# Kernel tuning notes

Hardware: AMD Instinct MI355X
Metric: run time of the kernel (lower is better)

Reference implementation:

```python
import jax, jax.numpy as jnp
import numpy as np

B, SQ, SK, D, H, DFF, L = 8, 1024, 1024, 512, 8, 2048, 2
HD = D // H  # head dim = 64
EPS = 1e-5


def _ln(x, g, b):
    mu = jnp.mean(x, axis=-1, keepdims=True)
    var = jnp.mean((x - mu) ** 2, axis=-1, keepdims=True)
    return (x - mu) * jax.lax.rsqrt(var + EPS) * g + b


def setup_inputs() -> dict:
    key = jax.random.key(0)
    ks = jax.random.split(key, 16)
    std = 0.02
    inp = {
        'q': jax.random.normal(ks[0], (B, SQ, D), jnp.float32),
        'k': jax.random.normal(ks[1], (B, SK, D), jnp.float32),
        'v': jax.random.normal(ks[2], (B, SK, D), jnp.float32),
        # per-layer stacked params (weights stored [in, out])
        'WQ': jax.random.normal(ks[3], (L, D, D), jnp.float32) * std,
        'bQ': jnp.zeros((L, D), jnp.float32),
        'WK': jax.random.normal(ks[4], (L, D, D), jnp.float32) * std,
        'bK': jnp.zeros((L, D), jnp.float32),
        'WV': jax.random.normal(ks[5], (L, D, D), jnp.float32) * std,
        'bV': jnp.zeros((L, D), jnp.float32),
        'WO': jax.random.normal(ks[6], (L, D, D), jnp.float32) * std,
        'bO': jnp.zeros((L, D), jnp.float32),
        'Wf1': jax.random.normal(ks[7], (L, D, DFF), jnp.float32) * std,
        'bf1': jnp.zeros((L, DFF), jnp.float32),
        'Wf2': jax.random.normal(ks[8], (L, DFF, D), jnp.float32) * std,
        'bf2': jnp.zeros((L, D), jnp.float32),
        'ln1_g': jnp.ones((L, D), jnp.float32),
        'ln1_b': jnp.zeros((L, D), jnp.float32),
        'ln2_g': jnp.ones((L, D), jnp.float32),
        'ln2_b': jnp.zeros((L, D), jnp.float32),
        'scale': jnp.full((L,), HD ** -0.5, jnp.float32),       # self.scale init
        'extra_scale': jnp.ones((L,), jnp.float32),             # self.extra_scale init
        'gate_attn': jnp.ones((L,), jnp.float32),
        'gate_ffn': jnp.ones((L,), jnp.float32),
    }
    return inp


def reference(q, k, v, WQ, bQ, WK, bK, WV, bV, WO, bO, Wf1, bf1, Wf2, bf2,
              ln1_g, ln1_b, ln2_g, ln2_b, scale, extra_scale, gate_attn, gate_ffn):
    prev = None  # Realformer residual attention scores
    for i in range(L):
        # QKV projections -> [B, H, S, HD]
        qh = (jnp.einsum('bsd,de->bse', q, WQ[i]) + bQ[i]).reshape(B, SQ, H, HD).transpose(0, 2, 1, 3)
        kh = (jnp.einsum('bsd,de->bse', k, WK[i]) + bK[i]).reshape(B, SK, H, HD).transpose(0, 2, 1, 3)
        vh = (jnp.einsum('bsd,de->bse', v, WV[i]) + bV[i]).reshape(B, SK, H, HD).transpose(0, 2, 1, 3)
        eff_scale = scale[i] * jnp.clip(extra_scale[i], 0.01, 50.0)
        scores = jnp.einsum('bhqd,bhkd->bhqk', qh, kh) * eff_scale  # [B,H,SQ,SK]
        if prev is not None:
            scores = scores + prev
        attn = jax.nn.softmax(scores, axis=-1)
        out = jnp.einsum('bhqk,bhkd->bhqd', attn, vh)
        out = out.transpose(0, 2, 1, 3).reshape(B, SQ, D)
        out = jnp.einsum('bsd,de->bse', out, WO[i]) + bO[i]
        # gated residual + post-norm
        q = q + jax.nn.softplus(gate_attn[i]) * out
        q = _ln(q, ln1_g[i], ln1_b[i])
        # FFN (exact gelu like torch default)
        ff = jax.nn.gelu(jnp.einsum('bsd,df->bsf', q, Wf1[i]) + bf1[i], approximate=False)
        ff = jnp.einsum('bsf,fd->bsd', ff, Wf2[i]) + bf2[i]
        q = q + jax.nn.softplus(gate_ffn[i]) * ff
        q = _ln(q, ln2_g[i], ln2_b[i])
        prev = scores
    return q
```

## Files before the change

### kernel.cpp

```cpp
#include <hip/hip_runtime.h>

#define B_   8
#define SQ_  1024
#define SK_  1024
#define D_   512
#define H_   8
#define DFF_ 2048
#define L_   2
#define HD_  64
#define M_   8192

typedef __bf16 bf16;
using bf16x8 = __attribute__((ext_vector_type(8))) __bf16;
using f32x4  = __attribute__((ext_vector_type(4))) float;

__device__ inline f32x4 mfma16(bf16x8 a, bf16x8 b, f32x4 c) {
  return __builtin_amdgcn_mfma_f32_16x16x32_bf16(a, b, c, 0, 0, 0);
}

__device__ __forceinline__ void gl2lds16(const bf16* g, bf16* l) {
  __builtin_amdgcn_global_load_lds(
      (const __attribute__((address_space(1))) void*)g,
      (__attribute__((address_space(3))) void*)l, 16, 0, 0);
}

__device__ __forceinline__ float gelu_fast(float x) {
  float u = 1.5957691216f * (x + 0.044715f * x * x * x);
  return x / (1.0f + __expf(-u));
}

struct TP4 { const float* in[4]; bf16* out[4]; };
__global__ __launch_bounds__(256) void transpose4_k(TP4 p) {
  __shared__ bf16 tile[32][33];
  int z = blockIdx.z, wsel = z >> 1, l = z & 1;
  const float* inp  = p.in[wsel]  + (size_t)l * D_ * D_;
  bf16*        outp = p.out[wsel] + (size_t)l * D_ * D_;
  int c0 = blockIdx.x * 32, r0 = blockIdx.y * 32;
  int tx = threadIdx.x & 31, ty = threadIdx.x >> 5;
#pragma unroll
  for (int i = 0; i < 32; i += 8)
    tile[ty + i][tx] = (bf16)inp[(size_t)(r0 + ty + i) * D_ + c0 + tx];
  __syncthreads();
#pragma unroll
  for (int i = 0; i < 32; i += 8)
    outp[(size_t)(c0 + ty + i) * D_ + r0 + tx] = tile[tx][ty + i];
}

__global__ __launch_bounds__(256) void transpose_k(
    const float* __restrict__ in, bf16* __restrict__ out, int R, int C) {
  __shared__ bf16 tile[32][33];
  const float* inp  = in  + (size_t)blockIdx.z * R * C;
  bf16*        outp = out + (size_t)blockIdx.z * R * C;
  int c0 = blockIdx.x * 32, r0 = blockIdx.y * 32;
  int tx = threadIdx.x & 31, ty = threadIdx.x >> 5;
#pragma unroll
  for (int i = 0; i < 32; i += 8)
    tile[ty + i][tx] = (bf16)inp[(size_t)(r0 + ty + i) * C + c0 + tx];
  __syncthreads();
#pragma unroll
  for (int i = 0; i < 32; i += 8)
    outp[(size_t)(c0 + ty + i) * R + r0 + tx] = tile[tx][ty + i];
}

__global__ __launch_bounds__(256) void f2b3_k(
    const float* __restrict__ a, const float* __restrict__ b,
    const float* __restrict__ c, bf16* __restrict__ oa,
    bf16* __restrict__ ob, bf16* __restrict__ oc) {
  int which = blockIdx.y;
  const float* in = (which == 0) ? a : (which == 1) ? b : c;
  bf16* out = (which == 0) ? oa : (which == 1) ? ob : oc;
  int i = (blockIdx.x * 256 + threadIdx.x) * 4;
  float4 v = *(const float4*)&in[i];
  out[i] = (bf16)v.x; out[i + 1] = (bf16)v.y;
  out[i + 2] = (bf16)v.z; out[i + 3] = (bf16)v.w;
}

struct G256 { const bf16* A; const bf16* Bt; const float* bias; bf16* C; };

#define MFB(mh) \
  _Pragma("unroll") \
  for (int mi = 0; mi < 4; mi++) { \
    _Pragma("unroll") \
    for (int ni = 0; ni < 4; ni++) \
      acc[(mh) * 4 + mi][ni] = mfma16(a[mi], b[ni], acc[(mh) * 4 + mi][ni]); \
  }

#define PHASE(s, mh, STAGE, VM) \
  { \
    if ((mh) == 0) { \
      a[0] = ldA(s, 0); a[1] = ldA(s, 1); a[2] = ldA(s, 2); a[3] = ldA(s, 3); \
      b[0] = ldB(s, 0); b[1] = ldB(s, 1); b[2] = ldB(s, 2); b[3] = ldB(s, 3); \
    } else { \
      a[0] = ldA(s, 4); a[1] = ldA(s, 5); a[2] = ldA(s, 6); a[3] = ldA(s, 7); \
    } \
    STAGE; \
    VM; \
    __builtin_amdgcn_s_barrier(); \
    asm volatile("s_waitcnt lgkmcnt(0)" ::: "memory"); \
    __builtin_amdgcn_sched_barrier(0); \
    __builtin_amdgcn_s_setprio(1); \
    MFB(mh); \
    __builtin_amdgcn_s_setprio(0); \
    __builtin_amdgcn_s_barrier(); \
  }

__global__ __launch_bounds__(512, 2) void gemm256_k(G256 g0, G256 g1,
                                                    int Nsz, int Ksz,
                                                    int gelu) {
  __shared__ bf16 As[4 * 8192];
  __shared__ bf16 Bs[4 * 8192];
  const G256 g = blockIdx.z ? g1 : g0;
  const int tid = threadIdx.x;
  const int w = tid >> 6, lane = tid & 63;
  const int quad = lane >> 4, l16 = lane & 15;
  const int wm = w >> 2, wn = w & 3;
  const int m0 = blockIdx.x * 256, n0 = blockIdx.y * 256;
  const int NCH = Ksz >> 5;
  const int ITERS = NCH >> 2;

  const int srow = tid >> 2;
  const int ssw = ((tid & 3) ^ (srow & 3) ^ ((srow >> 2) & 3)) << 3;
  const int swr = ((quad ^ (l16 & 3) ^ (l16 >> 2)) << 3);

  auto stageA = [&](int kc, int s) {
    const bf16* gp = g.A + (size_t)(m0 + srow) * Ksz + kc * 32 + ssw;
    gl2lds16(gp, &As[s * 8192 + w * 512]);
    gl2lds16(gp + (size_t)128 * Ksz, &As[s * 8192 + 4096 + w * 512]);
  };
  auto stageB = [&](int kc, int s) {
    const bf16* gp = g.Bt + (size_t)(n0 + srow) * Ksz + kc * 32 + ssw;
    gl2lds16(gp, &Bs[s * 8192 + w * 512]);
    gl2lds16(gp + (size_t)128 * Ksz, &Bs[s * 8192 + 4096 + w * 512]);
  };
  auto ldA = [&](int s, int mi) {
    return *(const bf16x8*)&As[s * 8192 + (wm * 128 + mi * 16 + l16) * 32 + swr];
  };
  auto ldB = [&](int s, int ni) {
    return *(const bf16x8*)&Bs[s * 8192 + (wn * 64 + ni * 16 + l16) * 32 + swr];
  };

  f32x4 acc[8][4] = {};

  stageA(0, 0); stageB(0, 0);
  stageA(1, 1); stageB(1, 1);
  stageA(2, 2); stageB(2, 2);
  asm volatile("s_waitcnt vmcnt(4)" ::: "memory");
  __builtin_amdgcn_s_barrier();

  for (int it = 0; it < ITERS; ++it) {
    const int c = it * 4;
    const bool last = (it + 1 == ITERS);
    bf16x8 a[4], b[4];
    PHASE(0, 0, stageA(c + 3, 3), )
    PHASE(0, 1, stageB(c + 3, 3), )
    PHASE(1, 0, if (!last) stageA(c + 4, 0), )
    PHASE(1, 1, if (!last) stageB(c + 4, 0),
          if (!last) { asm volatile("s_waitcnt vmcnt(4)" ::: "memory"); }
          else { asm volatile("s_waitcnt vmcnt(0)" ::: "memory"); })
    PHASE(2, 0, if (!last) stageA(c + 5, 1), )
    PHASE(2, 1, if (!last) stageB(c + 5, 1), )
    PHASE(3, 0, if (!last) stageA(c + 6, 2), )
    PHASE(3, 1, if (!last) stageB(c + 6, 2),
          asm volatile("s_waitcnt vmcnt(4)" ::: "memory"))
  }

#pragma unroll
  for (int mi = 0; mi < 8; mi++)
#pragma unroll
    for (int ni = 0; ni < 4; ni++) {
      const int col = n0 + wn * 64 + ni * 16 + l16;
      const float bv = g.bias[col];
#pragma unroll
      for (int r = 0; r < 4; r++) {
        const int row = m0 + wm * 128 + mi * 16 + quad * 4 + r;
        float x = acc[mi][ni][r] + bv;
        if (gelu) x = gelu_fast(x);
        g.C[(size_t)row * Nsz + col] = (bf16)x;
      }
    }
}

__global__ __launch_bounds__(512, 2) void gemm256s_k(
    const bf16* __restrict__ A, const bf16* __restrict__ Bt,
    bf16* __restrict__ P, int Nsz, int Kstride, int Kpart) {
  __shared__ bf16 As[4 * 8192];
  __shared__ bf16 Bs[4 * 8192];
  const int z = blockIdx.z;
  const int koff = z * Kpart;
  const int tid = threadIdx.x;
  const int w = tid >> 6, lane = tid & 63;
  const int quad = lane >> 4, l16 = lane & 15;
  const int wm = w >> 2, wn = w & 3;
  const int m0 = blockIdx.x * 256, n0 = blockIdx.y * 256;
  const int ITERS = (Kpart >> 5) >> 2;

  const int srow = tid >> 2;
  const int ssw = ((tid & 3) ^ (srow & 3) ^ ((srow >> 2) & 3)) << 3;
  const int swr = ((quad ^ (l16 & 3) ^ (l16 >> 2)) << 3);

  auto stageA = [&](int kc, int s) {
    const bf16* gp = A + (size_t)(m0 + srow) * Kstride + koff + kc * 32 + ssw;
    gl2lds16(gp, &As[s * 8192 + w * 512]);
    gl2lds16(gp + (size_t)128 * Kstride, &As[s * 8192 + 4096 + w * 512]);
  };
  auto stageB = [&](int kc, int s) {
    const bf16* gp = Bt + (size_t)(n0 + srow) * Kstride + koff + kc * 32 + ssw;
    gl2lds16(gp, &Bs[s * 8192 + w * 512]);
    gl2lds16(gp + (size_t)128 * Kstride, &Bs[s * 8192 + 4096 + w * 512]);
  };
  auto ldA = [&](int s, int mi) {
    return *(const bf16x8*)&As[s * 8192 + (wm * 128 + mi * 16 + l16) * 32 + swr];
  };
  auto ldB = [&](int s, int ni) {
    return *(const bf16x8*)&Bs[s * 8192 + (wn * 64 + ni * 16 + l16) * 32 + swr];
  };

  f32x4 acc[8][4] = {};

  stageA(0, 0); stageB(0, 0);
  stageA(1, 1); stageB(1, 1);
  stageA(2, 2); stageB(2, 2);
  asm volatile("s_waitcnt vmcnt(4)" ::: "memory");
  __builtin_amdgcn_s_barrier();

  for (int it = 0; it < ITERS; ++it) {
    const int c = it * 4;
    const bool last = (it + 1 == ITERS);
    bf16x8 a[4], b[4];
    PHASE(0, 0, stageA(c + 3, 3), )
    PHASE(0, 1, stageB(c + 3, 3), )
    PHASE(1, 0, if (!last) stageA(c + 4, 0), )
    PHASE(1, 1, if (!last) stageB(c + 4, 0),
          if (!last) { asm volatile("s_waitcnt vmcnt(4)" ::: "memory"); }
          else { asm volatile("s_waitcnt vmcnt(0)" ::: "memory"); })
    PHASE(2, 0, if (!last) stageA(c + 5, 1), )
    PHASE(2, 1, if (!last) stageB(c + 5, 1), )
    PHASE(3, 0, if (!last) stageA(c + 6, 2), )
    PHASE(3, 1, if (!last) stageB(c + 6, 2),
          asm volatile("s_waitcnt vmcnt(4)" ::: "memory"))
  }

  const size_t Msz = (size_t)gridDim.x * 256;
  bf16* Pz = P + (size_t)z * Msz * Nsz;
#pragma unroll
  for (int mi = 0; mi < 8; mi++)
#pragma unroll
    for (int ni = 0; ni < 4; ni++) {
      const int col = n0 + wn * 64 + ni * 16 + l16;
#pragma unroll
      for (int r = 0; r < 4; r++) {
        const int row = m0 + wm * 128 + mi * 16 + quad * 4 + r;
        Pz[(size_t)row * Nsz + col] = (bf16)acc[mi][ni][r];
      }
    }
}

__global__ __launch_bounds__(512, 2) void gemm128_k(
    const bf16* __restrict__ A, const bf16* __restrict__ Bt,
    const float* __restrict__ bias, bf16* __restrict__ Cb,
    float* __restrict__ Cf, int Nsz, int Ksz) {
  __shared__ bf16 As[4 * 4096];
  __shared__ bf16 Bs[4 * 4096];
  const int tid = threadIdx.x;
  const int w = tid >> 6, lane = tid & 63;
  const int quad = lane >> 4, l16 = lane & 15;
  const int wm = w >> 2, wn = w & 3;
  const int m0 = blockIdx.x * 128, n0 = blockIdx.y * 128;
  const int NCH = Ksz >> 5;

  const int srow = tid >> 2;
  const int ssw = ((tid & 3) ^ (srow & 3) ^ ((srow >> 2) & 3)) << 3;
  const int swr = ((quad ^ (l16 & 3) ^ (l16 >> 2)) << 3);

  auto stageChunk = [&](int kc) {
    const int s = kc & 3;
    gl2lds16(A + (size_t)(m0 + srow) * Ksz + kc * 32 + ssw,
             &As[s * 4096 + w * 512]);
    gl2lds16(Bt + (size_t)(n0 + srow) * Ksz + kc * 32 + ssw,
             &Bs[s * 4096 + w * 512]);
  };
  auto ldA = [&](int s, int mi) {
    return *(const bf16x8*)&As[s * 4096 + (wm * 64 + mi * 16 + l16) * 32 + swr];
  };
  auto ldB = [&](int s, int ni) {
    return *(const bf16x8*)&Bs[s * 4096 + (wn * 32 + ni * 16 + l16) * 32 + swr];
  };

  f32x4 acc[4][2] = {};

  stageChunk(0); stageChunk(1); stageChunk(2);
  asm volatile("s_waitcnt vmcnt(4)" ::: "memory");
  __builtin_amdgcn_s_barrier();

  auto phase = [&](int c, int vml) {
    const int s = c & 3;
    if (vml == 4) stageChunk(c + 3);
    bf16x8 a0 = ldA(s, 0), a1 = ldA(s, 1), a2 = ldA(s, 2), a3 = ldA(s, 3);
    bf16x8 b0 = ldB(s, 0), b1 = ldB(s, 1);
    if (vml == 4)      asm volatile("s_waitcnt vmcnt(4)" ::: "memory");
    else if (vml == 2) asm volatile("s_waitcnt vmcnt(2)" ::: "memory");
    else if (vml == 0) asm volatile("s_waitcnt vmcnt(0)" ::: "memory");
    __builtin_amdgcn_s_barrier();
    asm volatile("s_waitcnt lgkmcnt(0)" ::: "memory");
    __builtin_amdgcn_sched_barrier(0);
    __builtin_amdgcn_s_setprio(1);
    acc[0][0] = mfma16(a0, b0, acc[0][0]);
    acc[0][1] = mfma16(a0, b1, acc[0][1]);
    acc[1][0] = mfma16(a1, b0, acc[1][0]);
    acc[1][1] = mfma16(a1, b1, acc[1][1]);
    acc[2][0] = mfma16(a2, b0, acc[2][0]);
    acc[2][1] = mfma16(a2, b1, acc[2][1]);
    acc[3][0] = mfma16(a3, b0, acc[3][0]);
    acc[3][1] = mfma16(a3, b1, acc[3][1]);
    __builtin_amdgcn_s_setprio(0);
    __builtin_amdgcn_s_barrier();
  };

  for (int c = 0; c + 4 <= NCH; ++c) phase(c, 4);
  phase(NCH - 3, 2);
  phase(NCH - 2, 0);
  phase(NCH - 1, -1);

#pragma unroll
  for (int mi = 0; mi < 4; mi++)
#pragma unroll
    for (int ni = 0; ni < 2; ni++) {
      const int col = n0 + wn * 32 + ni * 16 + l16;
      const float bv = bias[col];
#pragma unroll
      for (int r = 0; r < 4; r++) {
        const int row = m0 + wm * 64 + mi * 16 + quad * 4 + r;
        float x = acc[mi][ni][r] + bv;
        size_t idx = (size_t)row * Nsz + col;
        if (Cb) Cb[idx] = (bf16)x;
        if (Cf) Cf[idx] = x;
      }
    }
}

__global__ __launch_bounds__(256) void vtrans2_k(const bf16* __restrict__ vhh,
                                                 bf16* __restrict__ vt0,
                                                 bf16* __restrict__ vt1) {
  __shared__ bf16 sm[64][72];
  int kt = blockIdx.x, bh = blockIdx.y, z = blockIdx.z;
  int coloff = z ? D_ : 0;
  bf16* vt = z ? vt1 : vt0;
  int b = bh >> 3, h = bh & 7;
  int tid = threadIdx.x;
  for (int c = tid; c < 512; c += 256) {
    int key = c >> 3, off = (c & 7) * 8;
    *(uint4*)&sm[key][off] = *(const uint4*)
        &vhh[(size_t)(b * SK_ + kt * 64 + key) * (2 * D_) + coloff + h * 64 + off];
  }
  __syncthreads();
  for (int c = tid; c < 512; c += 256) {
    int hd = c >> 3, koff = (c & 7) * 8;
    bf16 tmp[8];
#pragma unroll
    for (int j = 0; j < 8; j++) tmp[j] = sm[koff + j][hd];
    *(uint4*)&vt[(size_t)(bh * 64 + hd) * SK_ + kt * 64 + koff] = *(uint4*)tmp;
  }
}

template<bool HAS0>
__global__ __launch_bounds__(256) void attn_t(
    const bf16* __restrict__ qh, const bf16* __restrict__ qh0,
    const bf16* __restrict__ kh, const bf16* __restrict__ kh0, int kstride,
    const bf16* __restrict__ vt, const float* __restrict__ scale,
    const float* __restrict__ extra, int li, bf16* __restrict__ ctx) {
  __shared__ bf16 Ks[2 * 2 * 2048];
  __shared__ bf16 K0s[HAS0 ? 2 * 2 * 2048 : 64];
  __shared__ bf16 Vs[2 * 2 * 2048];
  __shared__ bf16 Ps[4][16 * 72];
  int qt = blockIdx.x, bh = blockIdx.y;
  int b = bh >> 3, h = bh & 7;
  int tid = threadIdx.x, w = tid >> 6, lane = tid & 63;
  int quad = lane >> 4, l16 = lane & 15;
  const int r4 = lane >> 2;
  const int c4s = (((lane & 3) ^ (r4 & 3) ^ ((r4 >> 2) & 3))) * 8;
  const int swr = ((quad ^ (l16 & 3) ^ (l16 >> 2)) << 3);
  float eff1 = scale[li] * fminf(fmaxf(extra[li], 0.01f), 50.0f);
  float eff0 = HAS0 ? scale[li - 1] * fminf(fmaxf(extra[li - 1], 0.01f), 50.0f) : 0.f;
  bf16x8 aq[2][2], aq0[2][2];
#pragma unroll
  for (int mi = 0; mi < 2; mi++) {
    int qrow = b * SQ_ + qt * 128 + w * 32 + mi * 16 + l16;
    const bf16* qp = qh + (size_t)qrow * D_ + h * 64 + quad * 8;
    aq[mi][0] = *(const bf16x8*)qp; aq[mi][1] = *(const bf16x8*)(qp + 32);
#pragma unroll
    for (int k2 = 0; k2 < 2; k2++)
#pragma unroll
      for (int j = 0; j < 8; j++)
        aq[mi][k2][j] = (bf16)((float)aq[mi][k2][j] * eff1);
    if constexpr (HAS0) {
      const bf16* qp0 = qh0 + (size_t)qrow * D_ + h * 64 + quad * 8;
      aq0[mi][0] = *(const bf16x8*)qp0; aq0[mi][1] = *(const bf16x8*)(qp0 + 32);
#pragma unroll
      for (int k2 = 0; k2 < 2; k2++)
#pragma unroll
        for (int j = 0; j < 8; j++)
          aq0[mi][k2][j] = (bf16)((float)aq0[mi][k2][j] * eff0);
    }
  }
  bf16x8 ones;
#pragma unroll
  for (int j = 0; j < 8; j++) ones[j] = (bf16)1.0f;

  f32x4 o[2][4] = {};
  f32x4 ol[2] = {};

  auto stage = [&](int kt, int bufi) {
    size_t kg = (size_t)(b * SK_ + kt * 64 + w * 16 + r4) * kstride + h * 64 + c4s;
    gl2lds16(&kh[kg],      &Ks[(bufi * 2 + 0) * 2048 + (w * 16) * 32]);
    gl2lds16(&kh[kg + 32], &Ks[(bufi * 2 + 1) * 2048 + (w * 16) * 32]);
    if constexpr (HAS0) {
      gl2lds16(&kh0[kg],      &K0s[(bufi * 2 + 0) * 2048 + (w * 16) * 32]);
      gl2lds16(&kh0[kg + 32], &K0s[(bufi * 2 + 1) * 2048 + (w * 16) * 32]);
    }
    size_t vg = (size_t)(bh * 64 + w * 16 + r4) * SK_ + kt * 64 + c4s;
    gl2lds16(&vt[vg],      &Vs[(bufi * 2 + 0) * 2048 + (w * 16) * 32]);
    gl2lds16(&vt[vg + 32], &Vs[(bufi * 2 + 1) * 2048 + (w * 16) * 32]);
  };

  stage(0, 0);
  __syncthreads();
  int buf = 0;
  for (int kt = 0; kt < SK_ / 64; kt++, buf ^= 1) {
    if (kt + 1 < SK_ / 64) stage(kt + 1, buf ^ 1);
    bf16x8 bv[2][4];
#pragma unroll
    for (int kk = 0; kk < 2; kk++)
#pragma unroll
      for (int ni = 0; ni < 4; ni++)
        bv[kk][ni] = *(const bf16x8*)&Vs[kk * 2048 + buf * 4096 +
                                         (ni * 16 + l16) * 32 + swr];
#pragma unroll
    for (int mi = 0; mi < 2; mi++) {
#pragma unroll
      for (int ni = 0; ni < 4; ni++) {
        int ro = (ni * 16 + l16) * 32 + swr;
        f32x4 t = {};
        __builtin_amdgcn_s_setprio(1);
        t = mfma16(aq[mi][0], *(const bf16x8*)&Ks[0 * 2048 + buf * 4096 + ro], t);
        t = mfma16(aq[mi][1], *(const bf16x8*)&Ks[1 * 2048 + buf * 4096 + ro], t);
        if constexpr (HAS0) {
          t = mfma16(aq0[mi][0], *(const bf16x8*)&K0s[0 * 2048 + buf * 4096 + ro], t);
          t = mfma16(aq0[mi][1], *(const bf16x8*)&K0s[1 * 2048 + buf * 4096 + ro], t);
        }
        __builtin_amdgcn_s_setprio(0);
#pragma unroll
        for (int r = 0; r < 4; r++)
          Ps[w][(quad * 4 + r) * 72 + ni * 16 + l16] = (bf16)__expf(t[r]);
      }
#pragma unroll
      for (int kk = 0; kk < 2; kk++) {
        bf16x8 ap = *(const bf16x8*)&Ps[w][l16 * 72 + kk * 32 + quad * 8];
        __builtin_amdgcn_s_setprio(1);
        ol[mi] = mfma16(ap, ones, ol[mi]);
#pragma unroll
        for (int ni = 0; ni < 4; ni++)
          o[mi][ni] = mfma16(ap, bv[kk][ni], o[mi][ni]);
        __builtin_amdgcn_s_setprio(0);
      }
    }
    __syncthreads();
  }
#pragma unroll
  for (int mi = 0; mi < 2; mi++)
#pragma unroll
    for (int ni = 0; ni < 4; ni++)
#pragma unroll
      for (int r = 0; r < 4; r++) {
        int row = b * SQ_ + qt * 128 + w * 32 + mi * 16 + quad * 4 + r;
        ctx[(size_t)row * D_ + h * 64 + ni * 16 + l16] =
            (bf16)(o[mi][ni][r] / ol[mi][r]);
      }
}

__global__ __launch_bounds__(256) void ln_k(
    const float* __restrict__ cur_in, const float* __restrict__ add,
    const float* __restrict__ gate, const float* __restrict__ g,
    const float* __restrict__ bb, float* __restrict__ outf,
    bf16* __restrict__ outb) {
  int row = blockIdx.x, tid = threadIdx.x;
  float gv = gate[0];
  float sp = gv > 20.f ? gv : log1pf(expf(gv));
  size_t base = (size_t)row * D_;
  int c0 = tid * 2;
  float2 c2 = *(const float2*)&cur_in[base + c0];
  float2 a2 = *(const float2*)&add[base + c0];
  float x0 = c2.x + sp * a2.x, x1 = c2.y + sp * a2.y;
  float s = x0 + x1, s2 = x0 * x0 + x1 * x1;
#pragma unroll
  for (int m = 1; m < 64; m <<= 1) {
    s += __shfl_xor(s, m);
    s2 += __shfl_xor(s2, m);
  }
  __shared__ float sa[4], sb[4];
  int w = tid >> 6;
  if ((tid & 63) == 0) { sa[w] = s; sb[w] = s2; }
  __syncthreads();
  s = sa[0] + sa[1] + sa[2] + sa[3];
  s2 = sb[0] + sb[1] + sb[2] + sb[3];
  float mu = s * (1.f / D_);
  float var = s2 * (1.f / D_) - mu * mu;
  float rs = rsqrtf(var + 1e-5f);
  float y0 = (x0 - mu) * rs * g[c0] + bb[c0];
  float y1 = (x1 - mu) * rs * g[c0 + 1] + bb[c0 + 1];
  if (outf) { float2 y; y.x = y0; y.y = y1; *(float2*)&outf[base + c0] = y; }
  if (outb) { outb[base + c0] = (bf16)y0; outb[base + c0 + 1] = (bf16)y1; }
}

__global__ __launch_bounds__(256) void ln4_k(
    const float* __restrict__ cur_in, const bf16* __restrict__ P,
    const float* __restrict__ bias2, const float* __restrict__ gate,
    const float* __restrict__ g, const float* __restrict__ bb,
    float* __restrict__ outf, bf16* __restrict__ outb) {
  int row = blockIdx.x, tid = threadIdx.x;
  float gv = gate[0];
  float sp = gv > 20.f ? gv : log1pf(expf(gv));
  size_t base = (size_t)row * D_;
  int c0 = tid * 2;
  float2 c2 = *(const float2*)&cur_in[base + c0];
  float a0 = bias2[c0], a1 = bias2[c0 + 1];
  const size_t MD = (size_t)M_ * D_;
#pragma unroll
  for (int z = 0; z < 4; z++) {
    const bf16* pp = P + z * MD + base + c0;
    a0 += (float)pp[0];
    a1 += (float)pp[1];
  }
  float x0 = c2.x + sp * a0, x1 = c2.y + sp * a1;
  float s = x0 + x1, s2 = x0 * x0 + x1 * x1;
#pragma unroll
  for (int m = 1; m < 64; m <<= 1) {
    s += __shfl_xor(s, m);
    s2 += __shfl_xor(s2, m);
  }
  __shared__ float sa[4], sb[4];
  int w = tid >> 6;
  if ((tid & 63) == 0) { sa[w] = s; sb[w] = s2; }
  __syncthreads();
  s = sa[0] + sa[1] + sa[2] + sa[3];
  s2 = sb[0] + sb[1] + sb[2] + sb[3];
  float mu = s * (1.f / D_);
  float var = s2 * (1.f / D_) - mu * mu;
  float rs = rsqrtf(var + 1e-5f);
  float y0 = (x0 - mu) * rs * g[c0] + bb[c0];
  float y1 = (x1 - mu) * rs * g[c0 + 1] + bb[c0 + 1];
  if (outf) { float2 y; y.x = y0; y.y = y1; *(float2*)&outf[base + c0] = y; }
  if (outb) { outb[base + c0] = (bf16)y0; outb[base + c0 + 1] = (bf16)y1; }
}

extern "C" void kernel_launch(void* const* d_in, const int* in_sizes, int n_in,
                              void* d_out, int out_size, void* d_ws,
                              size_t ws_size, hipStream_t stream) {
  const float* qin = (const float*)d_in[0];
  const float* kin = (const float*)d_in[1];
  const float* vin = (const float*)d_in[2];
  const float* WQ  = (const float*)d_in[3];
  const float* bQ  = (const float*)d_in[4];
  const float* WK  = (const float*)d_in[5];
  const float* bK  = (const float*)d_in[6];
  const float* WV  = (const float*)d_in[7];
  const float* bV  = (const float*)d_in[8];
  const float* WO  = (const float*)d_in[9];
  const float* bO  = (const float*)d_in[10];
  const float* Wf1 = (const float*)d_in[11];
  const float* bf1 = (const float*)d_in[12];
  const float* Wf2 = (const float*)d_in[13];
  const float* bf2 = (const float*)d_in[14];
  const float* l1g = (const float*)d_in[15];
  const float* l1b = (const float*)d_in[16];
  const float* l2g = (const float*)d_in[17];
  const float* l2b = (const float*)d_in[18];
  const float* sc  = (const float*)d_in[19];
  const float* ex  = (const float*)d_in[20];
  const float* ga  = (const float*)d_in[21];
  const float* gf  = (const float*)d_in[22];

  char* p = (char*)d_ws;
  auto alloc = [&](size_t bytes) {
    void* r = (void*)p;
    p += (bytes + 255) & ~(size_t)255;
    return r;
  };
  bf16* WQt  = (bf16*)alloc((size_t)L_ * D_ * D_ * 2);
  bf16* WKt  = (bf16*)alloc((size_t)L_ * D_ * D_ * 2);
  bf16* WVt  = (bf16*)alloc((size_t)L_ * D_ * D_ * 2);
  bf16* WOt  = (bf16*)alloc((size_t)L_ * D_ * D_ * 2);
  bf16* Wf1t = (bf16*)alloc((size_t)L_ * D_ * DFF_ * 2);
  bf16* Wf2t = (bf16*)alloc((size_t)L_ * D_ * DFF_ * 2);
  float* cur  = (float*)alloc((size_t)M_ * D_ * 4);
  bf16* curb  = (bf16*)alloc((size_t)M_ * D_ * 2);
  bf16* qb    = (bf16*)alloc((size_t)M_ * D_ * 2);
  bf16* kb    = (bf16*)alloc((size_t)M_ * D_ * 2);
  bf16* vb    = (bf16*)alloc((size_t)M_ * D_ * 2);
  bf16* khh   = (bf16*)alloc((size_t)M_ * 2 * D_ * 2);
  bf16* vhh   = (bf16*)alloc((size_t)M_ * 2 * D_ * 2);
  bf16* qh0b  = (bf16*)alloc((size_t)M_ * D_ * 2);
  bf16* qh1b  = (bf16*)alloc((size_t)M_ * D_ * 2);
  bf16* vt0   = (bf16*)alloc((size_t)M_ * D_ * 2);
  bf16* vt1   = (bf16*)alloc((size_t)M_ * D_ * 2);
  bf16* ctx   = (bf16*)alloc((size_t)M_ * D_ * 2);
  float* proj  = (float*)alloc((size_t)M_ * D_ * 4);
  float* ffout = (float*)alloc((size_t)M_ * D_ * 4);
  bf16* parts  = (bf16*)proj;
  bf16* ffmid  = (bf16*)alloc((size_t)M_ * DFF_ * 2);
  (void)ffout;

  TP4 tp; tp.in[0] = WQ; tp.in[1] = WK; tp.in[2] = WV; tp.in[3] = WO;
  tp.out[0] = WQt; tp.out[1] = WKt; tp.out[2] = WVt; tp.out[3] = WOt;
  transpose4_k<<<dim3(16, 16, 8), 256, 0, stream>>>(tp);
  transpose_k<<<dim3(DFF_ / 32, D_ / 32, L_), 256, 0, stream>>>(Wf1, Wf1t, D_, DFF_);
  transpose_k<<<dim3(D_ / 32, DFF_ / 32, L_), 256, 0, stream>>>(Wf2, Wf2t, DFF_, D_);
  f2b3_k<<<dim3((M_ * D_) / 1024, 3), 256, 0, stream>>>(qin, kin, vin, qb, kb, vb);

  G256 gk; gk.A = kb; gk.Bt = WKt; gk.bias = bK; gk.C = khh;
  G256 gvv; gvv.A = vb; gvv.Bt = WVt; gvv.bias = bV; gvv.C = vhh;
  gemm256_k<<<dim3(M_ / 256, (2 * D_) / 256, 2), 512, 0, stream>>>(
      gk, gvv, 2 * D_, D_, 0);
  vtrans2_k<<<dim3(SK_ / 64, B_ * H_, 2), 256, 0, stream>>>(vhh, vt0, vt1);
  gemm128_k<<<dim3(M_ / 128, 4), 512, 0, stream>>>(
      qb, WQt, bQ, qh0b, nullptr, D_, D_);

  for (int li = 0; li < L_; li++) {
    if (li > 0)
      gemm128_k<<<dim3(M_ / 128, 4), 512, 0, stream>>>(
          curb, WQt + (size_t)li * D_ * D_, bQ + li * D_, qh1b, nullptr, D_, D_);
    if (li == 0)
      attn_t<false><<<dim3(SQ_ / 128, B_ * H_), 256, 0, stream>>>(
          qh0b, qh0b, khh, khh, 2 * D_, vt0, sc, ex, 0, ctx);
    else
      attn_t<true><<<dim3(SQ_ / 128, B_ * H_), 256, 0, stream>>>(
          qh1b, qh0b, khh + (size_t)li * D_, khh, 2 * D_, vt1, sc, ex, 1, ctx);
    gemm128_k<<<dim3(M_ / 128, 4), 512, 0, stream>>>(
        ctx, WOt + (size_t)li * D_ * D_, bO + li * D_, nullptr, proj, D_, D_);
    ln_k<<<M_, 256, 0, stream>>>((li == 0) ? qin : cur, proj, ga + li,
                                 l1g + li * D_, l1b + li * D_, cur, curb);
    G256 gf1; gf1.A = curb; gf1.Bt = Wf1t + (size_t)li * D_ * DFF_;
    gf1.bias = bf1 + li * DFF_; gf1.C = ffmid;
    gemm256_k<<<dim3(M_ / 256, DFF_ / 256, 1), 512, 0, stream>>>(
        gf1, gf1, DFF_, D_, 1);
    gemm256s_k<<<dim3(M_ / 256, D_ / 256, 4), 512, 0, stream>>>(
        ffmid, Wf2t + (size_t)li * DFF_ * D_, parts, D_, DFF_, DFF_ / 4);
    ln4_k<<<M_, 256, 0, stream>>>(cur, parts, bf2 + li * D_, gf + li,
                                  l2g + li * D_, l2b + li * D_,
                                  (li == L_ - 1) ? (float*)d_out : cur,
                                  (li == L_ - 1) ? nullptr : curb);
  }
}
```

Baseline: 506.7 us.

## Shrink attention tiles to 64 query rows and 32-key steps

The attention kernel now handles 64 query rows per block (16 per wave) instead of 128, and steps through keys 32 at a time instead of 64. This doubles the grid, halves per-wave accumulator registers, and cuts LDS use. The aim is higher occupancy and better CU fill. In exchange, K/V tiles are reused across fewer query rows, there are twice as many sync steps, the XOR swizzle is dropped (possible LDS bank conflicts), and the setprio hints are removed.

New measurement: 498.1 us. About the same (-1.7%).

```diff
diff --git a/kernel.cpp b/kernel.cpp
--- a/kernel.cpp
+++ b/kernel.cpp
@@ -368,113 +368,106 @@
     const bf16* __restrict__ kh, const bf16* __restrict__ kh0, int kstride,
     const bf16* __restrict__ vt, const float* __restrict__ scale,
     const float* __restrict__ extra, int li, bf16* __restrict__ ctx) {
-  __shared__ bf16 Ks[2 * 2 * 2048];
-  __shared__ bf16 K0s[HAS0 ? 2 * 2 * 2048 : 64];
-  __shared__ bf16 Vs[2 * 2 * 2048];
-  __shared__ bf16 Ps[4][16 * 72];
+  __shared__ bf16 Ks[2 * 2048];
+  __shared__ bf16 K0s[HAS0 ? 2 * 2048 : 64];
+  __shared__ bf16 Vs[2 * 2048];
+  __shared__ bf16 Ps[4][16 * 40];
   int qt = blockIdx.x, bh = blockIdx.y;
   int b = bh >> 3, h = bh & 7;
   int tid = threadIdx.x, w = tid >> 6, lane = tid & 63;
   int quad = lane >> 4, l16 = lane & 15;
-  const int r4 = lane >> 2;
-  const int c4s = (((lane & 3) ^ (r4 & 3) ^ ((r4 >> 2) & 3))) * 8;
-  const int swr = ((quad ^ (l16 & 3) ^ (l16 >> 2)) << 3);
+  const int rr = lane >> 2, c8 = (lane & 3) * 8;
   float eff1 = scale[li] * fminf(fmaxf(extra[li], 0.01f), 50.0f);
   float eff0 = HAS0 ? scale[li - 1] * fminf(fmaxf(extra[li - 1], 0.01f), 50.0f) : 0.f;
-  bf16x8 aq[2][2], aq0[2][2];
-#pragma unroll
-  for (int mi = 0; mi < 2; mi++) {
-    int qrow = b * SQ_ + qt * 128 + w * 32 + mi * 16 + l16;
+
+  bf16x8 aq[2], aq0[2];
+  {
+    int qrow = b * SQ_ + qt * 64 + w * 16 + l16;
     const bf16* qp = qh + (size_t)qrow * D_ + h * 64 + quad * 8;
-    aq[mi][0] = *(const bf16x8*)qp; aq[mi][1] = *(const bf16x8*)(qp + 32);
+    aq[0] = *(const bf16x8*)qp; aq[1] = *(const bf16x8*)(qp + 32);
 #pragma unroll
     for (int k2 = 0; k2 < 2; k2++)
 #pragma unroll
       for (int j = 0; j < 8; j++)
-        aq[mi][k2][j] = (bf16)((float)aq[mi][k2][j] * eff1);
+        aq[k2][j] = (bf16)((float)aq[k2][j] * eff1);
     if constexpr (HAS0) {
       const bf16* qp0 = qh0 + (size_t)qrow * D_ + h * 64 + quad * 8;
-      aq0[mi][0] = *(const bf16x8*)qp0; aq0[mi][1] = *(const bf16x8*)(qp0 + 32);
+      aq0[0] = *(const bf16x8*)qp0; aq0[1] = *(const bf16x8*)(qp0 + 32);
 #pragma unroll
       for (int k2 = 0; k2 < 2; k2++)
 #pragma unroll
         for (int j = 0; j < 8; j++)
-          aq0[mi][k2][j] = (bf16)((float)aq0[mi][k2][j] * eff0);
+          aq0[k2][j] = (bf16)((float)aq0[k2][j] * eff0);
     }
   }
   bf16x8 ones;
 #pragma unroll
   for (int j = 0; j < 8; j++) ones[j] = (bf16)1.0f;
 
-  f32x4 o[2][4] = {};
-  f32x4 ol[2] = {};
+  f32x4 o[4] = {};
+  f32x4 ol = {};
 
   auto stage = [&](int kt, int bufi) {
-    size_t kg = (size_t)(b * SK_ + kt * 64 + w * 16 + r4) * kstride + h * 64 + c4s;
-    gl2lds16(&kh[kg],      &Ks[(bufi * 2 + 0) * 2048 + (w * 16) * 32]);
-    gl2lds16(&kh[kg + 32], &Ks[(bufi * 2 + 1) * 2048 + (w * 16) * 32]);
-    if constexpr (HAS0) {
-      gl2lds16(&kh0[kg],      &K0s[(bufi * 2 + 0) * 2048 + (w * 16) * 32]);
-      gl2lds16(&kh0[kg + 32], &K0s[(bufi * 2 + 1) * 2048 + (w * 16) * 32]);
-    }
-    size_t vg = (size_t)(bh * 64 + w * 16 + r4) * SK_ + kt * 64 + c4s;
-    gl2lds16(&vt[vg],      &Vs[(bufi * 2 + 0) * 2048 + (w * 16) * 32]);
-    gl2lds16(&vt[vg + 32], &Vs[(bufi * 2 + 1) * 2048 + (w * 16) * 32]);
+#pragma unroll
+    for (int ui = 0; ui < (HAS0 ? 3 : 2); ui++) {
+      int u = w + ui * 4;
+      if (u < 4) {
+        int hf = u >> 1, g = u & 1;
+        gl2lds16(&kh[(size_t)(b * SK_ + kt * 32 + g * 16 + rr) * kstride +
+                     h * 64 + hf * 32 + c8],
+                 &Ks[bufi * 2048 + hf * 1024 + g * 512]);
+      } else if (HAS0 && u < 8) {
+        int uu = u - 4; int hf = uu >> 1, g = uu & 1;
+        gl2lds16(&kh0[(size_t)(b * SK_ + kt * 32 + g * 16 + rr) * kstride +
+                      h * 64 + hf * 32 + c8],
+                 &K0s[bufi * 2048 + hf * 1024 + g * 512]);
+      } else {
+        int g2 = u & 3;
+        gl2lds16(&vt[(size_t)(bh * 64 + g2 * 16 + rr) * SK_ + kt * 32 + c8],
+                 &Vs[bufi * 2048 + g2 * 512]);
+      }
+    }
   };
 
   stage(0, 0);
   __syncthreads();
   int buf = 0;
-  for (int kt = 0; kt < SK_ / 64; kt++, buf ^= 1) {
-    if (kt + 1 < SK_ / 64) stage(kt + 1, buf ^ 1);
-    bf16x8 bv[2][4];
-#pragma unroll
-    for (int kk = 0; kk < 2; kk++)
+  for (int kt = 0; kt < SK_ / 32; kt++, buf ^= 1) {
+    if (kt + 1 < SK_ / 32) stage(kt + 1, buf ^ 1);
+#pragma unroll
+    for (int ni = 0; ni < 2; ni++) {
+      int ro = (ni * 16 + l16) * 32 + quad * 8;
+      f32x4 t = {};
+      t = mfma16(aq[0], *(const bf16x8*)&Ks[buf * 2048 + ro], t);
+      t = mfma16(aq[1], *(const bf16x8*)&Ks[buf * 2048 + 1024 + ro], t);
+      if constexpr (HAS0) {
+        t = mfma16(aq0[0], *(const bf16x8*)&K0s[buf * 2048 + ro], t);
+        t = mfma16(aq0[1], *(const bf16x8*)&K0s[buf * 2048 + 1024 + ro], t);
+      }
+#pragma unroll
+      for (int r = 0; r < 4; r++)
+        Ps[w][(quad * 4 + r) * 40 + ni * 16 + l16] = (bf16)__expf(t[r]);
+    }
+    {
+      bf16x8 ap = *(const bf16x8*)&Ps[w][l16 * 40 + quad * 8];
+      ol = mfma16(ap, ones, ol);
 #pragma unroll
       for (int ni = 0; ni < 4; ni++)
-        bv[kk][ni] = *(const bf16x8*)&Vs[kk * 2048 + buf * 4096 +
-                                         (ni * 16 + l16) * 32 + swr];
-#pragma unroll
-    for (int mi = 0; mi < 2; mi++) {
-#pragma unroll
-      for (int ni = 0; ni < 4; ni++) {
-        int ro = (ni * 16 + l16) * 32 + swr;
-        f32x4 t = {};
-        __builtin_amdgcn_s_setprio(1);
-        t = mfma16(aq[mi][0], *(const bf16x8*)&Ks[0 * 2048 + buf * 4096 + ro], t);
-        t = mfma16(aq[mi][1], *(const bf16x8*)&Ks[1 * 2048 + buf * 4096 + ro], t);
-        if constexpr (HAS0) {
-          t = mfma16(aq0[mi][0], *(const bf16x8*)&K0s[0 * 2048 + buf * 4096 + ro], t);
-          t = mfma16(aq0[mi][1], *(const bf16x8*)&K0s[1 * 2048 + buf * 4096 + ro], t);
-        }
-        __builtin_amdgcn_s_setprio(0);
-#pragma unroll
-        for (int r = 0; r < 4; r++)
-          Ps[w][(quad * 4 + r) * 72 + ni * 16 + l16] = (bf16)__expf(t[r]);
-      }
-#pragma unroll
-      for (int kk = 0; kk < 2; kk++) {
-        bf16x8 ap = *(const bf16x8*)&Ps[w][l16 * 72 + kk * 32 + quad * 8];
-        __builtin_amdgcn_s_setprio(1);
-        ol[mi] = mfma16(ap, ones, ol[mi]);
-#pragma unroll
-        for (int ni = 0; ni < 4; ni++)
-          o[mi][ni] = mfma16(ap, bv[kk][ni], o[mi][ni]);
-        __builtin_amdgcn_s_setprio(0);
-      }
+        o[ni] = mfma16(ap,
+                       *(const bf16x8*)&Vs[buf * 2048 + (ni * 16 + l16) * 32 +
+                                           quad * 8],
+                       o[ni]);
     }
     __syncthreads();
   }
 #pragma unroll
-  for (int mi = 0; mi < 2; mi++)
-#pragma unroll
-    for (int ni = 0; ni < 4; ni++)
-#pragma unroll
-      for (int r = 0; r < 4; r++) {
-        int row = b * SQ_ + qt * 128 + w * 32 + mi * 16 + quad * 4 + r;
-        ctx[(size_t)row * D_ + h * 64 + ni * 16 + l16] =
-            (bf16)(o[mi][ni][r] / ol[mi][r]);
-      }
+  for (int ni = 0; ni < 4; ni++)
+#pragma unroll
+    for (int r = 0; r < 4; r++) {
+      int row = b * SQ_ + qt * 64 + w * 16 + quad * 4 + r;
+      ctx[(size_t)row * D_ + h * 64 + ni * 16 + l16] =
+          (bf16)(o[ni][r] / ol[r]);
+    }
 }
 
 __global__ __launch_bounds__(256) void ln_k(
@@ -629,10 +622,10 @@
       gemm128_k<<<dim3(M_ / 128, 4), 512, 0, stream>>>(
           curb, WQt + (size_t)li * D_ * D_, bQ + li * D_, qh1b, nullptr, D_, D_);
     if (li == 0)
-      attn_t<false><<<dim3(SQ_ / 128, B_ * H_), 256, 0, stream>>>(
+      attn_t<false><<<dim3(SQ_ / 64, B_ * H_), 256, 0, stream>>>(
           qh0b, qh0b, khh, khh, 2 * D_, vt0, sc, ex, 0, ctx);
     else
-      attn_t<true><<<dim3(SQ_ / 128, B_ * H_), 256, 0, stream>>>(
+      attn_t<true><<<dim3(SQ_ / 64, B_ * H_), 256, 0, stream>>>(
           qh1b, qh0b, khh + (size_t)li * D_, khh, 2 * D_, vt1, sc, ex, 1, ctx);
     gemm128_k<<<dim3(M_ / 128, 4), 512, 0, stream>>>(
         ctx, WOt + (size_t)li * D_ * D_, bO + li * D_, nullptr, proj, D_, D_);
```
